# Optimization experiments

Measured on AMD Instinct MI355X. Metric: run time of the kernel, lower is better.

## Reference

```python
import jax, jax.numpy as jnp
import numpy as np

B, T, IN, OUT = 32, 2048, 1024, 256
DT = 1.0
TAU_MIN, TAU_MAX = 15.0, 25.0


def setup_inputs() -> dict:
    key = jax.random.key(0)
    k1, k2, k3 = jax.random.split(key, 3)
    inputs = jax.random.normal(k1, (B, T, IN), dtype=jnp.float32)
    bound = float(np.sqrt(1.0 / IN))
    weight = jax.random.uniform(k2, (OUT, IN), minval=-bound, maxval=bound, dtype=jnp.float32)
    bias = jnp.zeros((OUT,), dtype=jnp.float32)
    tau = jax.random.uniform(k3, (OUT,), minval=TAU_MIN, maxval=TAU_MAX, dtype=jnp.float32)
    decay = jnp.exp(-DT / tau)  # per-channel leak alpha in (0,1)
    return {"inputs": inputs, "weight": weight, "bias": bias, "decay": decay}


def reference(inputs, weight, bias, decay):
    # Dense projection: [B,T,IN] @ [IN,OUT] -> [B,T,OUT]
    current = jnp.einsum("bti,oi->bto", inputs, weight) + bias
    # Leaky integrator: u_t = alpha * u_{t-1} + (1-alpha) * x_t, u_0 = 0
    one_minus = 1.0 - decay

    def step(u, x):  # u,x: [B,OUT]
        u = decay * u + one_minus * x
        return u, u

    u0 = jnp.zeros((inputs.shape[0], weight.shape[0]), dtype=current.dtype)
    _, us = jax.lax.scan(step, u0, jnp.swapaxes(current, 0, 1))  # [T,B,OUT]
    return jnp.swapaxes(us, 0, 1)  # [B,T,OUT]
```

## Files before the change

### kernel.cpp

```cpp
#include <hip/hip_runtime.h>

#define B_   32
#define T_   2048
#define IN_  1024
#define OUT_ 256
#define M_   (B_ * T_)

#define BM 128
#define BN 256
#define BK 32
#define SK 256
#define NSTEPS (IN_ / BK)
#define NSUP (IN_ / SK)
#define THREADS 512
#define TPB 16

#define LC 32
#define XPAD 264

#define ALDS_BYTES (BM * SK * 2)
#define BBUF_OFF(c) (ALDS_BYTES + (c) * (BN * BK * 2))
#define XT_BYTES (BM * XPAD * 2)
#define SMEM_BYTES (ALDS_BYTES + 3 * (BN * BK * 2))

typedef __attribute__((ext_vector_type(4))) float f32x4;
typedef __attribute__((ext_vector_type(8))) __bf16 bf16x8;

__device__ __forceinline__ unsigned int f2bf_pk(float a, float b) {
    unsigned int ua = __float_as_uint(a);
    unsigned int ub = __float_as_uint(b);
    ua = (ua + 0x7fffu + ((ua >> 16) & 1u)) >> 16;
    ub = (ub + 0x7fffu + ((ub >> 16) & 1u)) >> 16;
    return ua | (ub << 16);
}
__device__ __forceinline__ unsigned short f2bf1(float a) {
    unsigned int ua = __float_as_uint(a);
    return (unsigned short)((ua + 0x7fffu + ((ua >> 16) & 1u)) >> 16);
}
__device__ __forceinline__ float bf2f(unsigned short s) {
    return __uint_as_float((unsigned int)s << 16);
}

__device__ __forceinline__ void gload_lds16(const void* g, void* l) {
    __builtin_amdgcn_global_load_lds(
        (const __attribute__((address_space(1))) void*)g,
        (__attribute__((address_space(3))) void*)l, 16, 0, 0);
}

__global__ __launch_bounds__(256) void convert_w_init(const float* __restrict__ W,
                                                      unsigned short* __restrict__ Wb,
                                                      unsigned int* __restrict__ flags) {
    const int i = blockIdx.x * 256 + threadIdx.x;
    const float4 v = ((const float4*)W)[i];
    uint2 o;
    o.x = f2bf_pk(v.x, v.y);
    o.y = f2bf_pk(v.z, v.w);
    ((uint2*)Wb)[i] = o;
    if (blockIdx.x == 0) {
        flags[threadIdx.x] = 0u;
        flags[256 + threadIdx.x] = 0u;
        if (threadIdx.x == 0) flags[512] = 0u;
    }
}

__global__ __launch_bounds__(THREADS, 2) void fused_all(
    const float* __restrict__ A, const unsigned short* __restrict__ Wb,
    const float* __restrict__ bias, const float* __restrict__ decay,
    float* __restrict__ out, float* __restrict__ localend,
    unsigned int* __restrict__ flags) {
    __shared__ __align__(16) char smem[SMEM_BYTES];
    __shared__ int s_tk;

    const int tid  = threadIdx.x;
    const int lane = tid & 63;
    const int wid  = tid >> 6;
    const int wm   = wid >> 2;
    const int wn   = wid & 3;
    const int l15  = lane & 15;
    const int l4   = lane >> 4;

    if (tid == 0) s_tk = (int)atomicAdd(&flags[512], 1u);
    __syncthreads();
    const int p    = s_tk;
    const int jb   = p & (TPB - 1);
    const int base = p - jb;
    const int bm0  = p * BM;

    const unsigned short* gsrcB[2];
    int ldsBbase[2];
#pragma unroll
    for (int i = 0; i < 2; ++i) {
        const int q = (wid + i * 8) * 64 + lane;
        const int r = q >> 2;
        const int g = (q & 3) ^ (r & 3);
        gsrcB[i] = Wb + (size_t)r * IN_ + g * 8;
        ldsBbase[i] = (wid + i * 8) * 1024;
    }

    f32x4 acc[4][4] = {};
    float4 av[16];

    const float* aRow = A + (size_t)(bm0 + (wid << 4)) * IN_ + (lane << 2);

    auto issueA = [&](int s) {
        __builtin_amdgcn_sched_barrier(0);
#pragma unroll
        for (int j = 0; j < 16; ++j)
            av[j] = *(const float4*)(aRow + (size_t)j * IN_ + s * SK);
        __builtin_amdgcn_sched_barrier(0);
    };
    auto packA = [&]() {
#pragma unroll
        for (int j = 0; j < 16; ++j) {
            const int row = (wid << 4) + j;
            const int phys = (lane >> 1) ^ (row & 31);
            uint2 pk;
            pk.x = f2bf_pk(av[j].x, av[j].y);
            pk.y = f2bf_pk(av[j].z, av[j].w);
            *(uint2*)&smem[row * 512 + phys * 16 + (lane & 1) * 8] = pk;
        }
    };

    gload_lds16(gsrcB[0], smem + BBUF_OFF(0) + ldsBbase[0]);
    gload_lds16(gsrcB[1], smem + BBUF_OFF(0) + ldsBbase[1]);
    issueA(0);
    asm volatile("s_waitcnt vmcnt(0)" ::: "memory");
    __builtin_amdgcn_sched_barrier(0);
    packA();
    asm volatile("s_waitcnt lgkmcnt(0)" ::: "memory");
    __builtin_amdgcn_s_barrier();
    __builtin_amdgcn_sched_barrier(0);
    gload_lds16(gsrcB[0] + BK, smem + BBUF_OFF(1) + ldsBbase[0]);
    gload_lds16(gsrcB[1] + BK, smem + BBUF_OFF(1) + ldsBbase[1]);

    const unsigned short* Alds = (const unsigned short*)smem;

    for (int i = 0; i < NSTEPS; ++i) {
        const int k = i & 7;
        const int s = i >> 3;
        if (k == 0 && i) {
            asm volatile("s_waitcnt vmcnt(4)" ::: "memory");
            __builtin_amdgcn_sched_barrier(0);
            __builtin_amdgcn_s_barrier();
            __builtin_amdgcn_sched_barrier(0);
            packA();
            asm volatile("s_waitcnt lgkmcnt(0)" ::: "memory");
            __builtin_amdgcn_sched_barrier(0);
        }
        if (i == NSTEPS - 1) {
            asm volatile("s_waitcnt vmcnt(0)" ::: "memory");
        } else if (k >= 6 && s < NSUP - 1) {
            asm volatile("s_waitcnt vmcnt(18)" ::: "memory");
        } else {
            asm volatile("s_waitcnt vmcnt(2)" ::: "memory");
        }
        __builtin_amdgcn_sched_barrier(0);
        __builtin_amdgcn_s_barrier();
        __builtin_amdgcn_sched_barrier(0);
        if (i + 2 < NSTEPS) {
            const int k0 = (i + 2) * BK;
            const int sl = (i + 2) % 3;
            gload_lds16(gsrcB[0] + k0, smem + BBUF_OFF(sl) + ldsBbase[0]);
            gload_lds16(gsrcB[1] + k0, smem + BBUF_OFF(sl) + ldsBbase[1]);
        }
        if (k == 5 && s < NSUP - 1) issueA(s + 1);
        {
            const unsigned short* Bb = (const unsigned short*)(smem + BBUF_OFF(i % 3));
            bf16x8 af[4], bfv[4];
#pragma unroll
            for (int mi = 0; mi < 4; ++mi) {
                const int row = wm * 64 + mi * 16 + l15;
                const int g   = k * 4 + l4;
                af[mi] = *(const bf16x8*)&Alds[row * SK + ((g ^ (row & 31)) << 3)];
            }
#pragma unroll
            for (int ni = 0; ni < 4; ++ni) {
                const int col = wn * 64 + ni * 16 + l15;
                bfv[ni] = *(const bf16x8*)&Bb[col * BK + ((l4 ^ (col & 3)) << 3)];
            }
#pragma unroll
            for (int mi = 0; mi < 4; ++mi)
#pragma unroll
                for (int ni = 0; ni < 4; ++ni)
                    acc[mi][ni] = __builtin_amdgcn_mfma_f32_16x16x32_bf16(
                        af[mi], bfv[ni], acc[mi][ni], 0, 0, 0);
        }
    }
    __syncthreads();

    unsigned short* xt = (unsigned short*)smem;
    float* ceL = (float*)(smem + XT_BYTES);
    float* caL = ceL + 4 * OUT_;

#pragma unroll
    for (int ni = 0; ni < 4; ++ni) {
        const int col = wn * 64 + ni * 16 + l15;
        const float bv = bias[col];
#pragma unroll
        for (int mi = 0; mi < 4; ++mi) {
            const int r0 = wm * 64 + mi * 16 + (l4 << 2);
#pragma unroll
            for (int r = 0; r < 4; ++r)
                xt[(r0 + r) * XPAD + col] = f2bf1(acc[mi][ni][r] + bv);
        }
    }
    __syncthreads();

    for (int task = tid; task < 4 * OUT_; task += THREADS) {
        const int cl  = task >> 8;
        const int col = task & 255;
        const float alpha = decay[col];
        const float om = 1.0f - alpha;
        float u = 0.0f;
        const unsigned short* px = &xt[(cl * LC) * XPAD + col];
#pragma unroll
        for (int t = 0; t < LC; ++t)
            u = fmaf(alpha, u, om * bf2f(px[t * XPAD]));
        ceL[cl * OUT_ + col] = u;
    }
    __syncthreads();

    float a32 = 0.f, a128 = 0.f;
    if (tid < OUT_) {
        const float alpha_c = decay[tid];
        a32 = alpha_c;
#pragma unroll
        for (int i = 1; i < LC; ++i) a32 *= alpha_c;
        const float t2 = a32 * a32;
        a128 = t2 * t2;
        float le = ceL[tid];
        le = fmaf(a32, le, ceL[OUT_ + tid]);
        le = fmaf(a32, le, ceL[2 * OUT_ + tid]);
        le = fmaf(a32, le, ceL[3 * OUT_ + tid]);
        __hip_atomic_store(&localend[(size_t)p * OUT_ + tid], le,
                           __ATOMIC_RELAXED, __HIP_MEMORY_SCOPE_AGENT);
    }
    __syncthreads();
    if (tid == 0)
        __hip_atomic_store(&flags[p], 1u, __ATOMIC_RELEASE, __HIP_MEMORY_SCOPE_AGENT);
    if (tid < jb) {
        while (__hip_atomic_load(&flags[base + tid], __ATOMIC_ACQUIRE,
                                 __HIP_MEMORY_SCOPE_AGENT) == 0u)
            __builtin_amdgcn_s_sleep(2);
    }
    __syncthreads();

    if (tid < OUT_) {
        float cin = 0.0f;
#pragma unroll
        for (int i = 0; i < TPB - 1; ++i) {
            float v = __hip_atomic_load(&localend[(size_t)(base + i) * OUT_ + tid],
                                        __ATOMIC_RELAXED, __HIP_MEMORY_SCOPE_AGENT);
            if (i < jb) cin = fmaf(a128, cin, v);
        }
        caL[tid] = cin;
        const float c1 = fmaf(a32, cin, ceL[tid]);
        const float c2 = fmaf(a32, c1, ceL[OUT_ + tid]);
        const float c3 = fmaf(a32, c2, ceL[2 * OUT_ + tid]);
        caL[OUT_ + tid] = c1;
        caL[2 * OUT_ + tid] = c2;
        caL[3 * OUT_ + tid] = c3;
    }
    __syncthreads();

    for (int task = tid; task < 4 * OUT_; task += THREADS) {
        const int cl  = task >> 8;
        const int col = task & 255;
        const float alpha = decay[col];
        const float om = 1.0f - alpha;
        float u = caL[cl * OUT_ + col];
        const unsigned short* px = &xt[(cl * LC) * XPAD + col];
        float* po = &out[(size_t)(bm0 + cl * LC) * OUT_ + col];
#pragma unroll
        for (int t = 0; t < LC; ++t) {
            u = fmaf(alpha, u, om * bf2f(px[t * XPAD]));
            po[(size_t)t * OUT_] = u;
        }
    }
}

__global__ __launch_bounds__(256) void gemm_bias(const float* __restrict__ A,
                                                 const float* __restrict__ W,
                                                 const float* __restrict__ bias,
                                                 float* __restrict__ C) {
    __shared__ float As[16][64 + 4];
    __shared__ float Ws[16][64 + 4];
    const int bm = blockIdx.y * 64;
    const int bn = blockIdx.x * 64;
    const int tid = threadIdx.x;
    const int tx = tid & 15, ty = tid >> 4;
    const int lr = tid >> 2, lc = (tid & 3) << 2;
    float acc[4][4] = {};
    const float* Ap = A + (size_t)(bm + lr) * IN_ + lc;
    const float* Wp = W + (size_t)(bn + lr) * IN_ + lc;
    for (int k0 = 0; k0 < IN_; k0 += 16) {
        const float4 a = *(const float4*)(Ap + k0);
        const float4 w = *(const float4*)(Wp + k0);
        __syncthreads();
        As[lc + 0][lr] = a.x; As[lc + 1][lr] = a.y; As[lc + 2][lr] = a.z; As[lc + 3][lr] = a.w;
        Ws[lc + 0][lr] = w.x; Ws[lc + 1][lr] = w.y; Ws[lc + 2][lr] = w.z; Ws[lc + 3][lr] = w.w;
        __syncthreads();
#pragma unroll
        for (int kk = 0; kk < 16; ++kk) {
            const float4 av = *(const float4*)&As[kk][ty << 2];
            const float4 wv = *(const float4*)&Ws[kk][tx << 2];
            const float a0[4] = {av.x, av.y, av.z, av.w};
            const float w0[4] = {wv.x, wv.y, wv.z, wv.w};
#pragma unroll
            for (int i = 0; i < 4; ++i)
#pragma unroll
                for (int j = 0; j < 4; ++j) acc[i][j] = fmaf(a0[i], w0[j], acc[i][j]);
        }
    }
#pragma unroll
    for (int i = 0; i < 4; ++i) {
        const size_t row = (size_t)(bm + (ty << 2) + i);
#pragma unroll
        for (int j = 0; j < 4; ++j)
            C[row * OUT_ + bn + (tx << 2) + j] = acc[i][j] + bias[bn + (tx << 2) + j];
    }
}

__global__ __launch_bounds__(OUT_) void scan_simple(float* __restrict__ C,
                                                    const float* __restrict__ decay) {
    const int b = blockIdx.x;
    const int o = threadIdx.x;
    const float alpha = decay[o];
    const float om = 1.0f - alpha;
    float u = 0.0f;
    float* p = C + (size_t)b * T_ * OUT_ + o;
    for (int t = 0; t < T_; ++t) {
        const float x = p[(size_t)t * OUT_];
        u = fmaf(alpha, u, om * x);
        p[(size_t)t * OUT_] = u;
    }
}

extern "C" void kernel_launch(void* const* d_in, const int* in_sizes, int n_in,
                              void* d_out, int out_size, void* d_ws, size_t ws_size,
                              hipStream_t stream) {
    const float* inputs = (const float*)d_in[0];
    const float* weight = (const float*)d_in[1];
    const float* bias   = (const float*)d_in[2];
    const float* decay  = (const float*)d_in[3];
    float* out = (float*)d_out;

    const size_t wb_bytes = (size_t)OUT_ * IN_ * 2;
    const size_t le_bytes = (size_t)(M_ / BM) * OUT_ * 4;
    const size_t fl_bytes = 4096;
    const size_t need = wb_bytes + le_bytes + fl_bytes;

    if (ws_size >= need) {
        char* w = (char*)d_ws;
        unsigned short* Wb  = (unsigned short*)w;
        float* localend     = (float*)(w + wb_bytes);
        unsigned int* flags = (unsigned int*)(w + wb_bytes + le_bytes);

        convert_w_init<<<(OUT_ * IN_ / 4) / 256, 256, 0, stream>>>(weight, Wb, flags);
        fused_all<<<M_ / BM, THREADS, 0, stream>>>(inputs, Wb, bias, decay,
                                                   out, localend, flags);
    } else {
        dim3 g(OUT_ / 64, M_ / 64);
        gemm_bias<<<g, 256, 0, stream>>>(inputs, weight, bias, out);
        scan_simple<<<B_, OUT_, 0, stream>>>(out, decay);
    }
}
```

Baseline: 137.7 us.

## Halve A super-tile depth and remap A loads to raise occupancy

The K depth of the A tile staged in LDS drops from 256 to 128, and the A load mapping changes to one row per four threads with contiguous 32-float chunks. Repacking moves to after the main barrier, and the XOR swizzle is adapted to the 16-group rows. Launch bounds now request 4 blocks per CU instead of 2, aiming to cut LDS and register use so more blocks overlap memory and compute. In exchange, A is repacked twice as often with more barriers, and registers per thread are tighter, which may cause spills.

```diff
diff --git a/kernel.cpp b/kernel.cpp
--- a/kernel.cpp
+++ b/kernel.cpp
@@ -9,7 +9,7 @@
 #define BM 128
 #define BN 256
 #define BK 32
-#define SK 256
+#define SK 128
 #define NSTEPS (IN_ / BK)
 #define NSUP (IN_ / SK)
 #define THREADS 512
@@ -63,13 +63,12 @@
     }
 }
 
-__global__ __launch_bounds__(THREADS, 2) void fused_all(
+__global__ __launch_bounds__(THREADS, 4) void fused_all(
     const float* __restrict__ A, const unsigned short* __restrict__ Wb,
     const float* __restrict__ bias, const float* __restrict__ decay,
     float* __restrict__ out, float* __restrict__ localend,
     unsigned int* __restrict__ flags) {
     __shared__ __align__(16) char smem[SMEM_BYTES];
-    __shared__ int s_tk;
 
     const int tid  = threadIdx.x;
     const int lane = tid & 63;
@@ -79,9 +78,10 @@
     const int l15  = lane & 15;
     const int l4   = lane >> 4;
 
-    if (tid == 0) s_tk = (int)atomicAdd(&flags[512], 1u);
-    __syncthreads();
-    const int p    = s_tk;
+    if (tid == 0) ((int*)smem)[0] = (int)atomicAdd(&flags[512], 1u);
+    __syncthreads();
+    const int p = ((int*)smem)[0];
+    __syncthreads();
     const int jb   = p & (TPB - 1);
     const int base = p - jb;
     const int bm0  = p * BM;
@@ -97,27 +97,31 @@
         ldsBbase[i] = (wid + i * 8) * 1024;
     }
 
+    const int rowA = tid >> 2;
+    const int cA   = tid & 3;
+    const float* aRow = A + (size_t)(bm0 + rowA) * IN_ + cA * 32;
+
     f32x4 acc[4][4] = {};
-    float4 av[16];
-
-    const float* aRow = A + (size_t)(bm0 + (wid << 4)) * IN_ + (lane << 2);
+    float4 av[8];
 
     auto issueA = [&](int s) {
         __builtin_amdgcn_sched_barrier(0);
 #pragma unroll
-        for (int j = 0; j < 16; ++j)
-            av[j] = *(const float4*)(aRow + (size_t)j * IN_ + s * SK);
+        for (int j = 0; j < 8; ++j)
+            av[j] = *(const float4*)(aRow + s * SK + j * 4);
         __builtin_amdgcn_sched_barrier(0);
     };
     auto packA = [&]() {
 #pragma unroll
-        for (int j = 0; j < 16; ++j) {
-            const int row = (wid << 4) + j;
-            const int phys = (lane >> 1) ^ (row & 31);
-            uint2 pk;
-            pk.x = f2bf_pk(av[j].x, av[j].y);
-            pk.y = f2bf_pk(av[j].z, av[j].w);
-            *(uint2*)&smem[row * 512 + phys * 16 + (lane & 1) * 8] = pk;
+        for (int m = 0; m < 4; ++m) {
+            const int g    = cA * 4 + m;
+            const int phys = g ^ (rowA & 15);
+            uint4 pk;
+            pk.x = f2bf_pk(av[2 * m].x,     av[2 * m].y);
+            pk.y = f2bf_pk(av[2 * m].z,     av[2 * m].w);
+            pk.z = f2bf_pk(av[2 * m + 1].x, av[2 * m + 1].y);
+            pk.w = f2bf_pk(av[2 * m + 1].z, av[2 * m + 1].w);
+            *(uint4*)&smem[rowA * 256 + phys * 16] = pk;
         }
     };
 
@@ -136,42 +140,39 @@
     const unsigned short* Alds = (const unsigned short*)smem;
 
     for (int i = 0; i < NSTEPS; ++i) {
-        const int k = i & 7;
-        const int s = i >> 3;
-        if (k == 0 && i) {
-            asm volatile("s_waitcnt vmcnt(4)" ::: "memory");
-            __builtin_amdgcn_sched_barrier(0);
-            __builtin_amdgcn_s_barrier();
-            __builtin_amdgcn_sched_barrier(0);
-            packA();
-            asm volatile("s_waitcnt lgkmcnt(0)" ::: "memory");
-            __builtin_amdgcn_sched_barrier(0);
-        }
+        const int k = i & 3;
+        const int s = i >> 2;
         if (i == NSTEPS - 1) {
             asm volatile("s_waitcnt vmcnt(0)" ::: "memory");
-        } else if (k >= 6 && s < NSUP - 1) {
-            asm volatile("s_waitcnt vmcnt(18)" ::: "memory");
+        } else if (k >= 2 && s < NSUP - 1) {
+            asm volatile("s_waitcnt vmcnt(10)" ::: "memory");
         } else {
             asm volatile("s_waitcnt vmcnt(2)" ::: "memory");
         }
         __builtin_amdgcn_sched_barrier(0);
         __builtin_amdgcn_s_barrier();
         __builtin_amdgcn_sched_barrier(0);
+        if (k == 0 && i) {
+            packA();
+            asm volatile("s_waitcnt lgkmcnt(0)" ::: "memory");
+            __builtin_amdgcn_s_barrier();
+            __builtin_amdgcn_sched_barrier(0);
+        }
         if (i + 2 < NSTEPS) {
             const int k0 = (i + 2) * BK;
             const int sl = (i + 2) % 3;
             gload_lds16(gsrcB[0] + k0, smem + BBUF_OFF(sl) + ldsBbase[0]);
             gload_lds16(gsrcB[1] + k0, smem + BBUF_OFF(sl) + ldsBbase[1]);
         }
-        if (k == 5 && s < NSUP - 1) issueA(s + 1);
+        if (k == 1 && s + 1 < NSUP) issueA(s + 1);
         {
             const unsigned short* Bb = (const unsigned short*)(smem + BBUF_OFF(i % 3));
             bf16x8 af[4], bfv[4];
+            const int kg = k * 4 + l4;
 #pragma unroll
             for (int mi = 0; mi < 4; ++mi) {
                 const int row = wm * 64 + mi * 16 + l15;
-                const int g   = k * 4 + l4;
-                af[mi] = *(const bf16x8*)&Alds[row * SK + ((g ^ (row & 31)) << 3)];
+                af[mi] = *(const bf16x8*)&Alds[row * SK + ((kg ^ (row & 15)) << 3)];
             }
 #pragma unroll
             for (int ni = 0; ni < 4; ++ni) {
```

New measurement: 190.5 us. +38.3%, slower.

## Double row tile to 256 with BK=64 double-buffered A/B and phased MFMA scheduling

Applied to the files above, without the earlier changes.

Doubles the M tile per block from 128 to 256 rows and the K step from 32 to 64. A is now staged through double-buffered bf16 LDS tiles with register prefetch, replacing the single 256-wide K super-stage, and B uses two rotating buffers with 128-byte swizzled rows. The MFMA work is split into four phases separated by barriers and s_setprio so LDS reads and global loads interleave with matrix ops. Each block reuses W across twice as many rows and the cross-block scan chain gets shorter, at the cost of half as many blocks, more accumulator registers per thread and a larger shared-memory footprint. Unseen grid and launch code must also halve the block count for the new tile size.

```diff
diff --git a/kernel.cpp b/kernel.cpp
--- a/kernel.cpp
+++ b/kernel.cpp
@@ -6,22 +6,21 @@
 #define OUT_ 256
 #define M_   (B_ * T_)
 
-#define BM 128
+#define BM 256
 #define BN 256
-#define BK 32
-#define SK 256
-#define NSTEPS (IN_ / BK)
-#define NSUP (IN_ / SK)
+#define BK 64
+#define NKT (IN_ / BK)
 #define THREADS 512
-#define TPB 16
+#define TPB (T_ / BM)
 
 #define LC 32
+#define NCHUNK (BM / LC)
 #define XPAD 264
 
-#define ALDS_BYTES (BM * SK * 2)
-#define BBUF_OFF(c) (ALDS_BYTES + (c) * (BN * BK * 2))
+#define ABUF_OFF(c) ((c) * 32768)
+#define BBUF_OFF(c) (65536 + (c) * 32768)
 #define XT_BYTES (BM * XPAD * 2)
-#define SMEM_BYTES (ALDS_BYTES + 3 * (BN * BK * 2))
+#define SMEM_BYTES (XT_BYTES + 2 * NCHUNK * OUT_ * 4)
 
 typedef __attribute__((ext_vector_type(4))) float f32x4;
 typedef __attribute__((ext_vector_type(8))) __bf16 bf16x8;
@@ -86,119 +85,158 @@
     const int base = p - jb;
     const int bm0  = p * BM;
 
-    const unsigned short* gsrcB[2];
-    int ldsBbase[2];
-#pragma unroll
-    for (int i = 0; i < 2; ++i) {
-        const int q = (wid + i * 8) * 64 + lane;
-        const int r = q >> 2;
-        const int g = (q & 3) ^ (r & 3);
-        gsrcB[i] = Wb + (size_t)r * IN_ + g * 8;
-        ldsBbase[i] = (wid + i * 8) * 1024;
-    }
-
-    f32x4 acc[4][4] = {};
-    float4 av[16];
-
-    const float* aRow = A + (size_t)(bm0 + (wid << 4)) * IN_ + (lane << 2);
-
-    auto issueA = [&](int s) {
-        __builtin_amdgcn_sched_barrier(0);
-#pragma unroll
-        for (int j = 0; j < 16; ++j)
-            av[j] = *(const float4*)(aRow + (size_t)j * IN_ + s * SK);
-        __builtin_amdgcn_sched_barrier(0);
+    const int rA = tid >> 1;
+    const int hA = tid & 1;
+    const float* gsrcA = A + (size_t)(bm0 + rA) * IN_ + hA * 32;
+
+    const unsigned short* gsrcBl[4];
+    int ldsBbase[4];
+#pragma unroll
+    for (int i = 0; i < 4; ++i) {
+        const int G = (wid * 4 + i) * 64 + lane;
+        const int r = G >> 3;
+        const int g = (G & 7) ^ (r & 7);
+        gsrcBl[i] = Wb + (size_t)r * IN_ + g * 8;
+        ldsBbase[i] = (wid * 4 + i) * 1024;
+    }
+
+    f32x4 acc[8][4] = {};
+    float4 av[8];
+
+    auto loadAv = [&](int kt) {
+#pragma unroll
+        for (int j = 0; j < 8; ++j)
+            av[j] = *(const float4*)(gsrcA + kt * BK + j * 4);
     };
-    auto packA = [&]() {
-#pragma unroll
-        for (int j = 0; j < 16; ++j) {
-            const int row = (wid << 4) + j;
-            const int phys = (lane >> 1) ^ (row & 31);
-            uint2 pk;
-            pk.x = f2bf_pk(av[j].x, av[j].y);
-            pk.y = f2bf_pk(av[j].z, av[j].w);
-            *(uint2*)&smem[row * 512 + phys * 16 + (lane & 1) * 8] = pk;
+    auto writeAv = [&](int buf) {
+#pragma unroll
+        for (int j2 = 0; j2 < 4; ++j2) {
+            uint4 pk;
+            pk.x = f2bf_pk(av[2 * j2].x,     av[2 * j2].y);
+            pk.y = f2bf_pk(av[2 * j2].z,     av[2 * j2].w);
+            pk.z = f2bf_pk(av[2 * j2 + 1].x, av[2 * j2 + 1].y);
+            pk.w = f2bf_pk(av[2 * j2 + 1].z, av[2 * j2 + 1].w);
+            const int g = hA * 4 + j2;
+            *(uint4*)&smem[ABUF_OFF(buf) + rA * 128 + ((g ^ (rA & 7)) << 4)] = pk;
         }
     };
 
-    gload_lds16(gsrcB[0], smem + BBUF_OFF(0) + ldsBbase[0]);
-    gload_lds16(gsrcB[1], smem + BBUF_OFF(0) + ldsBbase[1]);
-    issueA(0);
+#pragma unroll
+    for (int i = 0; i < 4; ++i) gload_lds16(gsrcBl[i],      smem + BBUF_OFF(0) + ldsBbase[i]);
+#pragma unroll
+    for (int i = 0; i < 4; ++i) gload_lds16(gsrcBl[i] + BK, smem + BBUF_OFF(1) + ldsBbase[i]);
+    loadAv(0);
     asm volatile("s_waitcnt vmcnt(0)" ::: "memory");
     __builtin_amdgcn_sched_barrier(0);
-    packA();
+    writeAv(0);
+    loadAv(1);
+    asm volatile("s_waitcnt vmcnt(0)" ::: "memory");
+    __builtin_amdgcn_sched_barrier(0);
+    writeAv(1);
+    loadAv(2);
     asm volatile("s_waitcnt lgkmcnt(0)" ::: "memory");
     __builtin_amdgcn_s_barrier();
     __builtin_amdgcn_sched_barrier(0);
-    gload_lds16(gsrcB[0] + BK, smem + BBUF_OFF(1) + ldsBbase[0]);
-    gload_lds16(gsrcB[1] + BK, smem + BBUF_OFF(1) + ldsBbase[1]);
-
-    const unsigned short* Alds = (const unsigned short*)smem;
-
-    for (int i = 0; i < NSTEPS; ++i) {
-        const int k = i & 7;
-        const int s = i >> 3;
-        if (k == 0 && i) {
+
+#define LOAD_AF(q)                                                              \
+    {                                                                           \
+        _Pragma("unroll")                                                       \
+        for (int j = 0; j < 2; ++j) {                                           \
+            _Pragma("unroll")                                                   \
+            for (int ks = 0; ks < 2; ++ks) {                                    \
+                const int row = wm * 128 + (2 * (q) + j) * 16 + l15;            \
+                const int g   = ks * 4 + l4;                                    \
+                af[j][ks] = *(const bf16x8*)&smem[ABUF_OFF(cur) + row * 128 +   \
+                                                  ((g ^ (row & 7)) << 4)];      \
+            }                                                                   \
+        }                                                                       \
+    }
+#define MFMA_Q(q)                                                               \
+    {                                                                           \
+        _Pragma("unroll")                                                       \
+        for (int j = 0; j < 2; ++j) {                                           \
+            _Pragma("unroll")                                                   \
+            for (int ni = 0; ni < 4; ++ni) {                                    \
+                _Pragma("unroll")                                               \
+                for (int ks = 0; ks < 2; ++ks)                                  \
+                    acc[2 * (q) + j][ni] = __builtin_amdgcn_mfma_f32_16x16x32_bf16( \
+                        af[j][ks], bfr[ni][ks], acc[2 * (q) + j][ni], 0, 0, 0); \
+            }                                                                   \
+        }                                                                       \
+    }
+#define PHASE_MID()                                                             \
+    __builtin_amdgcn_s_barrier();                                               \
+    asm volatile("s_waitcnt lgkmcnt(0)" ::: "memory");                          \
+    __builtin_amdgcn_sched_barrier(0);                                          \
+    __builtin_amdgcn_s_setprio(1);
+#define PHASE_END()                                                             \
+    __builtin_amdgcn_s_setprio(0);                                              \
+    __builtin_amdgcn_s_barrier();
+
+    for (int kt = 0; kt < NKT; ++kt) {
+        const int cur = kt & 1;
+        const int kt2 = kt + 2;
+        const bool doB = (kt2 < NKT);
+        bf16x8 bfr[4][2];
+        bf16x8 af[2][2];
+#pragma unroll
+        for (int ni = 0; ni < 4; ++ni)
+#pragma unroll
+            for (int ks = 0; ks < 2; ++ks) {
+                const int col = wn * 64 + ni * 16 + l15;
+                const int g   = ks * 4 + l4;
+                bfr[ni][ks] = *(const bf16x8*)&smem[BBUF_OFF(cur) + col * 128 +
+                                                    ((g ^ (col & 7)) << 4)];
+            }
+        LOAD_AF(0)
+        PHASE_MID()
+        MFMA_Q(0)
+        PHASE_END()
+        LOAD_AF(1)
+        if (doB) {
+            gload_lds16(gsrcBl[0] + kt2 * BK, smem + BBUF_OFF(cur) + ldsBbase[0]);
+            gload_lds16(gsrcBl[1] + kt2 * BK, smem + BBUF_OFF(cur) + ldsBbase[1]);
+        }
+        PHASE_MID()
+        MFMA_Q(1)
+        PHASE_END()
+        LOAD_AF(2)
+        if (doB) gload_lds16(gsrcBl[2] + kt2 * BK, smem + BBUF_OFF(cur) + ldsBbase[2]);
+        PHASE_MID()
+        MFMA_Q(2)
+        PHASE_END()
+        LOAD_AF(3)
+        if (doB) gload_lds16(gsrcBl[3] + kt2 * BK, smem + BBUF_OFF(cur) + ldsBbase[3]);
+        __builtin_amdgcn_s_barrier();
+        asm volatile("s_waitcnt lgkmcnt(0)" ::: "memory");
+        __builtin_amdgcn_sched_barrier(0);
+        __builtin_amdgcn_s_setprio(1);
+        MFMA_Q(3)
+        __builtin_amdgcn_s_setprio(0);
+        if (kt <= NKT - 3) {
             asm volatile("s_waitcnt vmcnt(4)" ::: "memory");
-            __builtin_amdgcn_sched_barrier(0);
-            __builtin_amdgcn_s_barrier();
-            __builtin_amdgcn_sched_barrier(0);
-            packA();
-            asm volatile("s_waitcnt lgkmcnt(0)" ::: "memory");
-            __builtin_amdgcn_sched_barrier(0);
-        }
-        if (i == NSTEPS - 1) {
+        } else {
             asm volatile("s_waitcnt vmcnt(0)" ::: "memory");
-        } else if (k >= 6 && s < NSUP - 1) {
-            asm volatile("s_waitcnt vmcnt(18)" ::: "memory");
-        } else {
-            asm volatile("s_waitcnt vmcnt(2)" ::: "memory");
         }
         __builtin_amdgcn_sched_barrier(0);
         __builtin_amdgcn_s_barrier();
         __builtin_amdgcn_sched_barrier(0);
-        if (i + 2 < NSTEPS) {
-            const int k0 = (i + 2) * BK;
-            const int sl = (i + 2) % 3;
-            gload_lds16(gsrcB[0] + k0, smem + BBUF_OFF(sl) + ldsBbase[0]);
-            gload_lds16(gsrcB[1] + k0, smem + BBUF_OFF(sl) + ldsBbase[1]);
-        }
-        if (k == 5 && s < NSUP - 1) issueA(s + 1);
-        {
-            const unsigned short* Bb = (const unsigned short*)(smem + BBUF_OFF(i % 3));
-            bf16x8 af[4], bfv[4];
-#pragma unroll
-            for (int mi = 0; mi < 4; ++mi) {
-                const int row = wm * 64 + mi * 16 + l15;
-                const int g   = k * 4 + l4;
-                af[mi] = *(const bf16x8*)&Alds[row * SK + ((g ^ (row & 31)) << 3)];
-            }
-#pragma unroll
-            for (int ni = 0; ni < 4; ++ni) {
-                const int col = wn * 64 + ni * 16 + l15;
-                bfv[ni] = *(const bf16x8*)&Bb[col * BK + ((l4 ^ (col & 3)) << 3)];
-            }
-#pragma unroll
-            for (int mi = 0; mi < 4; ++mi)
-#pragma unroll
-                for (int ni = 0; ni < 4; ++ni)
-                    acc[mi][ni] = __builtin_amdgcn_mfma_f32_16x16x32_bf16(
-                        af[mi], bfv[ni], acc[mi][ni], 0, 0, 0);
-        }
+        if (kt2 < NKT) writeAv(cur);
+        if (kt + 3 < NKT) loadAv(kt + 3);
     }
     __syncthreads();
 
     unsigned short* xt = (unsigned short*)smem;
     float* ceL = (float*)(smem + XT_BYTES);
-    float* caL = ceL + 4 * OUT_;
+    float* caL = ceL + NCHUNK * OUT_;
 
 #pragma unroll
     for (int ni = 0; ni < 4; ++ni) {
         const int col = wn * 64 + ni * 16 + l15;
         const float bv = bias[col];
 #pragma unroll
-        for (int mi = 0; mi < 4; ++mi) {
-            const int r0 = wm * 64 + mi * 16 + (l4 << 2);
+        for (int mi = 0; mi < 8; ++mi) {
+            const int r0 = wm * 128 + mi * 16 + (l4 << 2);
 #pragma unroll
             for (int r = 0; r < 4; ++r)
                 xt[(r0 + r) * XPAD + col] = f2bf1(acc[mi][ni][r] + bv);
@@ -206,7 +244,7 @@
     }
     __syncthreads();
 
-    for (int task = tid; task < 4 * OUT_; task += THREADS) {
+    for (int task = tid; task < NCHUNK * OUT_; task += THREADS) {
         const int cl  = task >> 8;
         const int col = task & 255;
         const float alpha = decay[col];
@@ -220,18 +258,18 @@
     }
     __syncthreads();
 
-    float a32 = 0.f, a128 = 0.f;
+    float a32 = 0.f, a256 = 0.f;
     if (tid < OUT_) {
         const float alpha_c = decay[tid];
         a32 = alpha_c;
 #pragma unroll
         for (int i = 1; i < LC; ++i) a32 *= alpha_c;
-        const float t2 = a32 * a32;
-        a128 = t2 * t2;
+        float t2 = a32 * a32;
+        t2 = t2 * t2;
+        a256 = t2 * t2;
         float le = ceL[tid];
-        le = fmaf(a32, le, ceL[OUT_ + tid]);
-        le = fmaf(a32, le, ceL[2 * OUT_ + tid]);
-        le = fmaf(a32, le, ceL[3 * OUT_ + tid]);
+#pragma unroll
+        for (int c = 1; c < NCHUNK; ++c) le = fmaf(a32, le, ceL[c * OUT_ + tid]);
         __hip_atomic_store(&localend[(size_t)p * OUT_ + tid], le,
                            __ATOMIC_RELAXED, __HIP_MEMORY_SCOPE_AGENT);
     }
@@ -251,19 +289,19 @@
         for (int i = 0; i < TPB - 1; ++i) {
             float v = __hip_atomic_load(&localend[(size_t)(base + i) * OUT_ + tid],
                                         __ATOMIC_RELAXED, __HIP_MEMORY_SCOPE_AGENT);
-            if (i < jb) cin = fmaf(a128, cin, v);
+            if (i < jb) cin = fmaf(a256, cin, v);
         }
         caL[tid] = cin;
-        const float c1 = fmaf(a32, cin, ceL[tid]);
-        const float c2 = fmaf(a32, c1, ceL[OUT_ + tid]);
-        const float c3 = fmaf(a32, c2, ceL[2 * OUT_ + tid]);
-        caL[OUT_ + tid] = c1;
-        caL[2 * OUT_ + tid] = c2;
-        caL[3 * OUT_ + tid] = c3;
-    }
-    __syncthreads();
-
-    for (int task = tid; task < 4 * OUT_; task += THREADS) {
+        float c = cin;
+#pragma unroll
+        for (int k = 1; k < NCHUNK; ++k) {
+            c = fmaf(a32, c, ceL[(k - 1) * OUT_ + tid]);
+            caL[k * OUT_ + tid] = c;
+        }
+    }
+    __syncthreads();
+
+    for (int task = tid; task < NCHUNK * OUT_; task += THREADS) {
         const int cl  = task >> 8;
         const int col = task & 255;
         const float alpha = decay[col];
```

Result: faster. 118.1 us (-14.2%).
